# Kernel optimization log

Measured on AMD Instinct MI355X. Metric: run time of the kernel, lower is better.

Reference implementation:

```python
import jax, jax.numpy as jnp
import numpy as np

T, H, E, K, I = 8192, 1024, 8, 2, 512  # tokens, hidden, experts, top_k, expert_intermediate
IS = I * 1  # shared-expert intermediate = expert_intermediate_size * num_shared_experts


def setup_inputs() -> dict:
    key = jax.random.key(0)
    ks = jax.random.split(key, 6)
    s = lambda *d: 1.0 / np.sqrt(d[0])
    return {
        "hidden_states": jax.random.normal(ks[0], (T, H), dtype=jnp.float32),
        "w_gate": jax.random.normal(ks[1], (H, E), dtype=jnp.float32) * s(H),
        "w_experts_gate_up": jax.random.normal(ks[2], (E, H, 2 * I), dtype=jnp.float32) * s(H),
        "w_experts_down": jax.random.normal(ks[3], (E, I, H), dtype=jnp.float32) * s(I),
        "w_shared_gate_up": jax.random.normal(ks[4], (H, 2 * IS), dtype=jnp.float32) * s(H),
        "w_shared_down": jax.random.normal(ks[5], (IS, H), dtype=jnp.float32) * s(IS),
    }


def _silu_and_mul(gu):
    d = gu.shape[-1] // 2
    return jax.nn.silu(gu[..., :d]) * gu[..., d:]


def reference(hidden_states, w_gate, w_experts_gate_up, w_experts_down,
              w_shared_gate_up, w_shared_down):
    x = hidden_states  # [T, H]

    # shared expert: SwiGLU MLP (reduce_results=False path)
    shared_out = _silu_and_mul(x @ w_shared_gate_up) @ w_shared_down  # [T, H]

    # router gate + top-k with renormalization (norm_expert_prob=True)
    router_logits = x @ w_gate  # [T, E]
    probs = jax.nn.softmax(router_logits.astype(jnp.float32), axis=-1)
    topk_w, topk_idx = jax.lax.top_k(probs, K)  # [T, K]
    topk_w = topk_w / jnp.sum(topk_w, axis=-1, keepdims=True)
    # scatter top-k weights into a sparse [T, E] combine matrix
    full_w = jnp.zeros((T, E), dtype=x.dtype)
    full_w = full_w.at[jnp.arange(T)[:, None], topk_idx].set(topk_w.astype(x.dtype))

    # expert SwiGLU MLPs (grouped GEMM expressed as batched einsum over experts)
    gu = jnp.einsum('th,ehi->eti', x, w_experts_gate_up)       # [E, T, 2I]
    act = _silu_and_mul(gu)                                     # [E, T, I]
    expert_out = jnp.einsum('eti,eih->eth', act, w_experts_down)  # [E, T, H]

    # weighted combine over selected experts (weights are zero elsewhere)
    moe_out = jnp.einsum('te,eth->th', full_w, expert_out)     # [T, H]

    return moe_out + shared_out
```

## Files before the change

kernel.cpp:

```cpp
#include <hip/hip_runtime.h>
#include <hip/hip_bf16.h>
#include <cstdint>

#define T_TOK 8192
#define HID   1024
#define NE    9
#define ISZ   512
#define RBASE 18432
#define NSLOT (RBASE + T_TOK)

#define BM 256
#define NROWB (NSLOT / BM)

typedef unsigned short u16;
typedef unsigned int   u32;
typedef signed char    i8;
typedef __attribute__((ext_vector_type(8))) short short8;
typedef __attribute__((ext_vector_type(4))) float f32x4;
typedef __attribute__((ext_vector_type(4))) int   i32x4;

__device__ __forceinline__ u16 f2bf(float f) {
  u32 u = __builtin_bit_cast(u32, f);
  return (u16)((u + 0x7fffu + ((u >> 16) & 1u)) >> 16);
}
__device__ __forceinline__ float bf2f(u16 v) {
  return __builtin_bit_cast(float, (u32)v << 16);
}
__device__ __forceinline__ int q8(float v, float inv) {
  int q = (int)__builtin_rintf(v * inv);
  return (q > 127) ? 127 : ((q < -127) ? -127 : q);
}
__device__ __forceinline__ int colp_of(int c) {
  int i = (c < 512) ? c : (c - 512);
  return (i >> 4) * 32 + ((c < 512) ? 0 : 16) + (i & 15);
}

#define STAGE(gp, lp) __builtin_amdgcn_global_load_lds( \
    (__attribute__((address_space(1))) u32*)(gp),       \
    (__attribute__((address_space(3))) u32*)(lp), 16, 0, 0)

__global__ __launch_bounds__(256) void k_wamax_part(
    const float* __restrict__ wgu, const float* __restrict__ wsg,
    float* __restrict__ pmax) {
  const int e = blockIdx.y, hb = blockIdx.x;
  const float* src = (e < 8) ? (wgu + (size_t)e * 1048576) : wsg;
  const int wv = threadIdx.x >> 6, l = threadIdx.x & 63;
  float4 m4[4];
#pragma unroll
  for (int j = 0; j < 4; ++j) m4[j] = make_float4(0.f, 0.f, 0.f, 0.f);
  const int r0 = hb * 16 + wv * 4;
#pragma unroll
  for (int r = 0; r < 4; ++r) {
    const float* row = src + (size_t)(r0 + r) * 1024;
#pragma unroll
    for (int j = 0; j < 4; ++j) {
      const float4 v = *(const float4*)&row[j * 256 + l * 4];
      m4[j].x = fmaxf(m4[j].x, fabsf(v.x));
      m4[j].y = fmaxf(m4[j].y, fabsf(v.y));
      m4[j].z = fmaxf(m4[j].z, fabsf(v.z));
      m4[j].w = fmaxf(m4[j].w, fabsf(v.w));
    }
  }
  __shared__ float4 red[4][4][64];
#pragma unroll
  for (int j = 0; j < 4; ++j) red[wv][j][l] = m4[j];
  __syncthreads();
  const int j2 = threadIdx.x >> 6, l2 = threadIdx.x & 63;
  const float4 a = red[0][j2][l2], b = red[1][j2][l2];
  const float4 c = red[2][j2][l2], d = red[3][j2][l2];
  float4 o;
  o.x = fmaxf(fmaxf(a.x, b.x), fmaxf(c.x, d.x));
  o.y = fmaxf(fmaxf(a.y, b.y), fmaxf(c.y, d.y));
  o.z = fmaxf(fmaxf(a.z, b.z), fmaxf(c.z, d.z));
  o.w = fmaxf(fmaxf(a.w, b.w), fmaxf(c.w, d.w));
  *(float4*)&pmax[((size_t)e * 64 + hb) * 1024 + j2 * 256 + l2 * 4] = o;
}

__global__ __launch_bounds__(256) void k_wamax_red(
    const float* __restrict__ pmax, float* __restrict__ swc) {
  const int flat = blockIdx.x * 256 + threadIdx.x;
  const int e = flat >> 10, c = flat & 1023;
  float m = 0.f;
  for (int hb = 0; hb < 64; ++hb)
    m = fmaxf(m, pmax[((size_t)e * 64 + hb) * 1024 + c]);
  swc[e * 1024 + colp_of(c)] = m * (1.f / 127.f);
}

#define NB_WGUP (32 * 8 * NE)
#define NB_WDN  (32 * 4 * NE)
#define NB_RTR  (T_TOK / 4)

__global__ __launch_bounds__(256) void k_prep(
    const float* __restrict__ x, const float* __restrict__ wg,
    const float* __restrict__ wgu, const float* __restrict__ wsg,
    const float* __restrict__ wdn, const float* __restrict__ wsd,
    const float* __restrict__ swc,
    i8* __restrict__ xq, float* __restrict__ sxg,
    i8* __restrict__ wguq, u16* __restrict__ wdT,
    int* __restrict__ eidx, float2* __restrict__ wts) {
  __shared__ float tile[32][129];
  const int b = blockIdx.x;
  const int tid = threadIdx.x;

  if (b < NB_WGUP) {
    const int e = b / 256, rem = b % 256;
    const int c0 = (rem & 31) * 32, h0 = (rem >> 5) * 128;
    const float* src = (e < 8) ? (wgu + (size_t)e * HID * 1024) : wsg;
    const int hl = tid >> 1, cb = (tid & 1) * 16;
#pragma unroll
    for (int j = 0; j < 4; ++j) {
      const float4 v = *(const float4*)&src[(size_t)(h0 + hl) * 1024 + c0 + cb + j * 4];
      tile[cb + j * 4 + 0][hl] = v.x;
      tile[cb + j * 4 + 1][hl] = v.y;
      tile[cb + j * 4 + 2][hl] = v.z;
      tile[cb + j * 4 + 3][hl] = v.w;
    }
    __syncthreads();
    const int cl = tid >> 3, hb = (tid & 7) * 16;
    const int cp = colp_of(c0 + cl);
    const float inv = 1.f / swc[e * 1024 + cp];
    i8 out[16];
#pragma unroll
    for (int k = 0; k < 16; ++k) out[k] = (i8)q8(tile[cl][hb + k], inv);
    *(int4*)&wguq[((size_t)e * 1024 + cp) * 1024 + h0 + hb] = *(int4*)out;
    return;
  }
  if (b < NB_WGUP + NB_WDN) {
    const int bb = b - NB_WGUP;
    const int e = bb / 128, r2 = bb % 128;
    const int h0 = (r2 & 31) * 32, i0 = (r2 >> 5) * 128;
    const float* src = (e < 8) ? (wdn + (size_t)e * ISZ * HID) : wsd;
    const int il = tid >> 1, hb2 = (tid & 1) * 16;
#pragma unroll
    for (int j = 0; j < 4; ++j) {
      const float4 v = *(const float4*)&src[(size_t)(i0 + il) * 1024 + h0 + hb2 + j * 4];
      tile[hb2 + j * 4 + 0][il] = v.x;
      tile[hb2 + j * 4 + 1][il] = v.y;
      tile[hb2 + j * 4 + 2][il] = v.z;
      tile[hb2 + j * 4 + 3][il] = v.w;
    }
    __syncthreads();
    const int hl2 = tid >> 3, ib = (tid & 7) * 16;
    u16 ob[16];
#pragma unroll
    for (int k = 0; k < 16; ++k) ob[k] = f2bf(tile[hl2][ib + k]);
    u16* dst = &wdT[((size_t)e * HID + h0 + hl2) * ISZ + i0 + ib];
    *(int4*)dst = *(int4*)ob;
    *(int4*)(dst + 8) = *(int4*)(ob + 8);
    return;
  }
  const int t = (b - NB_WGUP - NB_WDN) * 4 + (tid >> 6);
  const int l = tid & 63;
  float a[8] = {0, 0, 0, 0, 0, 0, 0, 0};
  float vals[16];
  float am = 0.f;
  const float4* xr4 = (const float4*)(x + (size_t)t * HID);
#pragma unroll
  for (int j = 0; j < 4; ++j) {
    const float4 v = xr4[j * 64 + l];
    vals[4 * j] = v.x; vals[4 * j + 1] = v.y; vals[4 * j + 2] = v.z; vals[4 * j + 3] = v.w;
    am = fmaxf(am, fmaxf(fmaxf(fabsf(v.x), fabsf(v.y)), fmaxf(fabsf(v.z), fabsf(v.w))));
    const int h = (j * 64 + l) * 4;
#pragma unroll
    for (int i = 0; i < 4; ++i) {
      const float4 w0 = *(const float4*)&wg[(h + i) * 8];
      const float4 w1 = *(const float4*)&wg[(h + i) * 8 + 4];
      const float ev = vals[4 * j + i];
      a[0] += ev * w0.x; a[1] += ev * w0.y; a[2] += ev * w0.z; a[3] += ev * w0.w;
      a[4] += ev * w1.x; a[5] += ev * w1.y; a[6] += ev * w1.z; a[7] += ev * w1.w;
    }
  }
#pragma unroll
  for (int off = 32; off >= 1; off >>= 1) {
    am = fmaxf(am, __shfl_xor(am, off));
#pragma unroll
    for (int e2 = 0; e2 < 8; ++e2) a[e2] += __shfl_xor(a[e2], off);
  }
  const float inv = (am > 0.f) ? 127.f / am : 0.f;
  u32* xq4 = (u32*)(xq + (size_t)t * HID);
#pragma unroll
  for (int j = 0; j < 4; ++j) {
    u32 q = ((u32)(unsigned char)(i8)q8(vals[4 * j], inv)) |
            ((u32)(unsigned char)(i8)q8(vals[4 * j + 1], inv) << 8) |
            ((u32)(unsigned char)(i8)q8(vals[4 * j + 2], inv) << 16) |
            ((u32)(unsigned char)(i8)q8(vals[4 * j + 3], inv) << 24);
    xq4[j * 64 + l] = q;
  }
  if (l == 0) {
    sxg[t] = am * (1.f / 127.f);
    int ia = 0;
#pragma unroll
    for (int e2 = 1; e2 < 8; ++e2) if (a[e2] > a[ia]) ia = e2;
    int ib = (ia == 0) ? 1 : 0;
#pragma unroll
    for (int e2 = 0; e2 < 8; ++e2) if (e2 != ia && a[e2] > a[ib]) ib = e2;
    float wa = 1.f / (1.f + expf(a[ib] - a[ia]));
    eidx[t] = ia | (ib << 8);
    wts[t] = make_float2(wa, 1.f - wa);
  }
}

__global__ __launch_bounds__(512) void k_scatter(
    const int* __restrict__ eidx, int* __restrict__ btok, int* __restrict__ slotmap,
    int* __restrict__ seg, int* __restrict__ segcnt) {
  __shared__ int cnt_s[8];
  __shared__ int goff_s[9];
  const int e = threadIdx.x >> 6;
  const int l = threadIdx.x & 63;

  int c1 = 0;
  for (int c = 0; c < T_TOK / 64; ++c) {
    int v = eidx[c * 64 + l];
    c1 += __popcll(__ballot((v & 255) == e)) + __popcll(__ballot(((v >> 8) & 255) == e));
  }
  if (l == 0) cnt_s[e] = c1;
  __syncthreads();
  if (threadIdx.x == 0) {
    int off = 0;
    for (int k = 0; k < 8; ++k) { goff_s[k] = off; off += (cnt_s[k] + 255) & ~255; }
    goff_s[8] = off;
  }
  __syncthreads();
  const int base0 = goff_s[e];
  const int cnt_e = cnt_s[e];
  const unsigned long long below = (l == 63) ? ~0ull >> 1 : ((1ull << l) - 1);

  int base = base0;
  for (int c = 0; c < T_TOK / 64; ++c) {
    const int t = c * 64 + l;
    const int v = eidx[t];
    const unsigned long long ma = __ballot((v & 255) == e);
    const unsigned long long mb = __ballot(((v >> 8) & 255) == e);
    if ((v & 255) == e) {
      int s = base + __popcll(ma & below);
      btok[s] = t; slotmap[2 * t] = s;
    }
    if (((v >> 8) & 255) == e) {
      int s = base + __popcll(ma) + __popcll(mb & below);
      btok[s] = t; slotmap[2 * t + 1] = s;
    }
    base += __popcll(ma) + __popcll(mb);
  }
  for (int p = cnt_e + l; p < ((cnt_e + 255) & ~255); p += 64) btok[base0 + p] = 0;
  if (threadIdx.x < 9) seg[threadIdx.x] = goff_s[threadIdx.x];
  if (threadIdx.x < 8) segcnt[threadIdx.x] = cnt_s[threadIdx.x];
}

__device__ __forceinline__ bool seg_lookup(const int* __restrict__ seg,
                                           const int* __restrict__ segcnt,
                                           int brow, int& e) {
  if (brow >= RBASE) { e = 8; return true; }
  if (brow >= seg[8]) return false;
  e = 0;
#pragma unroll
  for (int k = 1; k < 8; ++k) if (brow >= seg[k]) e = k;
  return brow < seg[e] + segcnt[e];
}


#define G1_STG(kt) do { const int _r = ((kt) & 1) * 32768;          \
    STAGE(sA0 + (kt) * 128, Ab + _r + 0 * 8192 + w * 1024);         \
    STAGE(sA1 + (kt) * 128, Ab + _r + 1 * 8192 + w * 1024);         \
    STAGE(sA2 + (kt) * 128, Ab + _r + 2 * 8192 + w * 1024);         \
    STAGE(sA3 + (kt) * 128, Ab + _r + 3 * 8192 + w * 1024);         \
    STAGE(sB0 + (kt) * 128, Bb + _r + 0 * 8192 + w * 1024);         \
    STAGE(sB1 + (kt) * 128, Bb + _r + 1 * 8192 + w * 1024);         \
    STAGE(sB2 + (kt) * 128, Bb + _r + 2 * 8192 + w * 1024);         \
    STAGE(sB3 + (kt) * 128, Bb + _r + 3 * 8192 + w * 1024); } while (0)

#define G1_LOADF(RG, KX) do {                                       \
    _Pragma("unroll") for (int m = 0; m < 4; ++m)                   \
      fA[m] = *(const i32x4*)&Ab[(RG) * 32768 + aBase + m * 2048 + (KX)]; \
    _Pragma("unroll") for (int n = 0; n < 8; ++n)                   \
      fB[n] = *(const i32x4*)&Bb[(RG) * 32768 + bBase + n * 2048 + (KX)]; } while (0)

#define G1_MFMA do { __builtin_amdgcn_s_setprio(1);                 \
    _Pragma("unroll") for (int m = 0; m < 4; ++m)                   \
      _Pragma("unroll") for (int n = 0; n < 8; ++n)                 \
        acc[m][n] = __builtin_amdgcn_mfma_i32_16x16x64_i8(fA[m], fB[n], acc[m][n], 0, 0, 0); \
    __builtin_amdgcn_s_setprio(0); } while (0)

__global__ __launch_bounds__(512) void k_gemm_gu(
    const i8* __restrict__ xq,
    const i8* __restrict__ wguq,
    const int* __restrict__ seg, const int* __restrict__ segcnt,
    const int* __restrict__ btok, const float* __restrict__ sxg,
    const float* __restrict__ swc,
    u16* __restrict__ act)
{
  const int bid = blockIdx.x;
  const int brow = (bid % NROWB) * BM;
  const int bcol = (bid / NROWB) * 256;
  int e;
  if (!seg_lookup(seg, segcnt, brow, e)) return;

  __shared__ __align__(16) i8 Ab[2 * 32768];
  __shared__ __align__(16) i8 Bb[2 * 32768];
  __shared__ float sxl[BM];
  __shared__ float swcl[256];

  const int tid = threadIdx.x;
  const int w = tid >> 6, l = tid & 63;
  const int wm = w >> 1, wn = w & 1;
  const int fr = l & 15, fg = l >> 4;

  if (tid < BM) {
    const int rrow = brow + tid;
    const int tk = (e < 8) ? btok[rrow] : (rrow - RBASE);
    sxl[tid] = sxg[tk];
  } else {
    swcl[tid - 256] = swc[e * 1024 + bcol + (tid - 256)];
  }

  const int rr = w * 8 + (l >> 3);
  const int sw = ((l & 7) ^ (l >> 3)) * 16;
  int tr[4];
#pragma unroll
  for (int j = 0; j < 4; ++j) {
    const int gr = brow + j * 64 + rr;
    tr[j] = (e < 8) ? btok[gr] : (gr - RBASE);
  }
  const i8* sA0 = xq + (size_t)tr[0] * HID + sw;
  const i8* sA1 = xq + (size_t)tr[1] * HID + sw;
  const i8* sA2 = xq + (size_t)tr[2] * HID + sw;
  const i8* sA3 = xq + (size_t)tr[3] * HID + sw;
  const i8* sB0 = wguq + ((size_t)e * 1024 + bcol + 0 * 64 + rr) * HID + sw;
  const i8* sB1 = wguq + ((size_t)e * 1024 + bcol + 1 * 64 + rr) * HID + sw;
  const i8* sB2 = wguq + ((size_t)e * 1024 + bcol + 2 * 64 + rr) * HID + sw;
  const i8* sB3 = wguq + ((size_t)e * 1024 + bcol + 3 * 64 + rr) * HID + sw;

  const int aBase = (wm * 64 + fr) * 128;
  const int bBase = (wn * 128 + fr) * 128;
  const int kx0 = (fg ^ (fr & 7)) * 16;
  const int kx1 = kx0 ^ 64;

  i32x4 acc[4][8];
#pragma unroll
  for (int m = 0; m < 4; ++m)
#pragma unroll
    for (int n = 0; n < 8; ++n) acc[m][n] = (i32x4){0, 0, 0, 0};
  i32x4 fA[4], fB[8];

  const int NKT = HID / 128;
  G1_STG(0);
  asm volatile("s_waitcnt vmcnt(0)" ::: "memory");
  __builtin_amdgcn_s_barrier();
  for (int s = 0; s < NKT; ++s) {
    const int rg = s & 1;
    if (s + 1 < NKT) G1_STG(s + 1);
    G1_LOADF(rg, kx0);
    asm volatile("s_waitcnt lgkmcnt(0)" ::: "memory");
    __builtin_amdgcn_sched_barrier(0);
    G1_MFMA;
    G1_LOADF(rg, kx1);
    asm volatile("s_waitcnt lgkmcnt(0)" ::: "memory");
    __builtin_amdgcn_sched_barrier(0);
    G1_MFMA;
    asm volatile("s_waitcnt vmcnt(0)" ::: "memory");
    __builtin_amdgcn_s_barrier();
  }

#pragma unroll
  for (int m = 0; m < 4; ++m) {
#pragma unroll
    for (int p = 0; p < 4; ++p) {
      const i32x4 gI = acc[m][2 * p], uI = acc[m][2 * p + 1];
      const int col = ((bcol + wn * 128) >> 1) + p * 16 + fr;
      const float swg = swcl[wn * 128 + p * 32 + fr];
      const float swu = swcl[wn * 128 + p * 32 + 16 + fr];
#pragma unroll
      for (int r = 0; r < 4; ++r) {
        const int row_l = wm * 64 + m * 16 + fg * 4 + r;
        const float sx = sxl[row_l];
        const float gate = (float)gI[r] * (sx * swg);
        const float up   = (float)uI[r] * (sx * swu);
        const float sv = gate / (1.f + __expf(-gate));
        act[(size_t)(brow + row_l) * ISZ + col] = f2bf(sv * up);
      }
    }
  }
}


#define D_STGA(kt) do { const int _d = ((kt) % 3) * 8192 + w * 1024; \
    STAGE(dA0 + (kt) * 32, As + _d);                                 \
    STAGE(dA1 + (kt) * 32, As + _d + 512); } while (0)
#define D_STGB(kt) do { const int _d = ((kt) % 3) * 8192 + w * 1024; \
    STAGE(dB0 + (kt) * 32, Bs + _d);                                 \
    STAGE(dB1 + (kt) * 32, Bs + _d + 512); } while (0)
#define D_LDA4(sl, mb) do {                                          \
    af[0] = *(const short8*)&As[(sl) + aOff + ((mb) + 0) * 512];     \
    af[1] = *(const short8*)&As[(sl) + aOff + ((mb) + 1) * 512];     \
    af[2] = *(const short8*)&As[(sl) + aOff + ((mb) + 2) * 512];     \
    af[3] = *(const short8*)&As[(sl) + aOff + ((mb) + 3) * 512]; } while (0)
#define D_LDB4(sl) do {                                              \
    bf[0] = *(const short8*)&Bs[(sl) + bOff + 0 * 512];              \
    bf[1] = *(const short8*)&Bs[(sl) + bOff + 1 * 512];              \
    bf[2] = *(const short8*)&Bs[(sl) + bOff + 2 * 512];              \
    bf[3] = *(const short8*)&Bs[(sl) + bOff + 3 * 512]; } while (0)
#define D_MFMA16(mb) do { __builtin_amdgcn_s_setprio(1);             \
    _Pragma("unroll") for (int mm = 0; mm < 4; ++mm)                 \
      _Pragma("unroll") for (int nn = 0; nn < 4; ++nn)               \
        accf[(mb) + mm][nn] = __builtin_amdgcn_mfma_f32_16x16x32_bf16( \
            af[mm], bf[nn], accf[(mb) + mm][nn], 0, 0, 0);           \
    __builtin_amdgcn_s_setprio(0); } while (0)

__global__ __launch_bounds__(512) void k_gemm_down(
    const u16* __restrict__ act, const u16* __restrict__ wdT,
    const int* __restrict__ seg, const int* __restrict__ segcnt,
    u16* __restrict__ tmp) {
  const int brow = blockIdx.x * BM;
  const int bcol = blockIdx.y * 256;
  int e;
  if (!seg_lookup(seg, segcnt, brow, e)) return;

  __shared__ __align__(16) u16 As[3 * 8192];
  __shared__ __align__(16) u16 Bs[3 * 8192];

  const int tid = threadIdx.x;
  const int w = tid >> 6, l = tid & 63;
  const int wm = w >> 2, wn = w & 3;
  const int fr = l & 15, fg = l >> 4;

  const int arow0 = (w * 128 + l) >> 2;
  const int swd = ((l & 3) ^ (arow0 & 3)) * 8;
  const u16* dA0 = act + (size_t)(brow + arow0) * ISZ + swd;
  const u16* dA1 = act + (size_t)(brow + arow0 + 16) * ISZ + swd;
  const u16* dB0 = wdT + ((size_t)e * 1024 + bcol + arow0) * ISZ + swd;
  const u16* dB1 = wdT + ((size_t)e * 1024 + bcol + arow0 + 16) * ISZ + swd;

  const int aOff = (wm * 128 + fr) * 32 + ((fg ^ (fr & 3)) * 8);
  const int bOff = (wn * 64 + fr) * 32 + ((fg ^ (fr & 3)) * 8);

  f32x4 accf[8][4];
#pragma unroll
  for (int m = 0; m < 8; ++m)
#pragma unroll
    for (int n = 0; n < 4; ++n) accf[m][n] = (f32x4){0.f, 0.f, 0.f, 0.f};
  short8 af[4], bf[4];

  const int NKT = ISZ / 32;
  D_STGA(0); D_STGB(0); D_STGA(1); D_STGB(1);
  asm volatile("s_waitcnt vmcnt(4)" ::: "memory");
  __builtin_amdgcn_s_barrier();
  for (int kt = 0; kt < NKT; ++kt) {
    const int sl = (kt % 3) * 8192;
    D_LDA4(sl, 0); D_LDB4(sl);
    if (kt + 2 < NKT) D_STGA(kt + 2);
    __builtin_amdgcn_s_barrier();
    asm volatile("s_waitcnt lgkmcnt(0)" ::: "memory");
    __builtin_amdgcn_sched_barrier(0);
    D_MFMA16(0);
    __builtin_amdgcn_s_barrier();
    D_LDA4(sl, 4);
    if (kt + 2 < NKT) D_STGB(kt + 2);
    __builtin_amdgcn_s_barrier();
    asm volatile("s_waitcnt lgkmcnt(0)" ::: "memory");
    __builtin_amdgcn_sched_barrier(0);
    D_MFMA16(4);
    if (kt + 2 < NKT)      { asm volatile("s_waitcnt vmcnt(4)" ::: "memory"); }
    else if (kt + 1 < NKT) { asm volatile("s_waitcnt vmcnt(0)" ::: "memory"); }
    __builtin_amdgcn_s_barrier();
  }

#pragma unroll
  for (int m = 0; m < 8; ++m) {
#pragma unroll
    for (int r = 0; r < 4; ++r) {
      const int row = brow + wm * 128 + m * 16 + fg * 4 + r;
#pragma unroll
      for (int n = 0; n < 4; ++n) {
        const int col = bcol + wn * 64 + n * 16 + fr;
        tmp[(size_t)row * HID + col] = f2bf(accf[m][n][r]);
      }
    }
  }
}

__global__ __launch_bounds__(256) void k_combine(
    const u16* __restrict__ tmp, const int* __restrict__ slotmap,
    const float2* __restrict__ wts, float* __restrict__ out) {
  const int idx = blockIdx.x * 256 + threadIdx.x;
  const int t = idx >> 7;
  const int c = (idx & 127) << 3;
  const int s0 = slotmap[2 * t], s1 = slotmap[2 * t + 1];
  const float2 wv = wts[t];
  const short8 a = *(const short8*)(tmp + (size_t)s0 * HID + c);
  const short8 b = *(const short8*)(tmp + (size_t)s1 * HID + c);
  const short8 s = *(const short8*)(tmp + (size_t)(RBASE + t) * HID + c);
  float r[8];
#pragma unroll
  for (int j = 0; j < 8; ++j)
    r[j] = bf2f((u16)s[j]) + wv.x * bf2f((u16)a[j]) + wv.y * bf2f((u16)b[j]);
  float* po = out + (size_t)t * HID + c;
  *(float4*)po       = make_float4(r[0], r[1], r[2], r[3]);
  *(float4*)(po + 4) = make_float4(r[4], r[5], r[6], r[7]);
}

extern "C" void kernel_launch(void* const* d_in, const int* in_sizes, int n_in,
                              void* d_out, int out_size, void* d_ws, size_t ws_size,
                              hipStream_t stream) {
  const float* x   = (const float*)d_in[0];
  const float* wg  = (const float*)d_in[1];
  const float* wgu = (const float*)d_in[2];
  const float* wdn = (const float*)d_in[3];
  const float* wsg = (const float*)d_in[4];
  const float* wsd = (const float*)d_in[5];
  float* out = (float*)d_out;

  char* ws = (char*)d_ws;
  i8*  xq    = (i8*)ws;   ws += (size_t)T_TOK * HID;
  i8*  wguq  = (i8*)ws;   ws += (size_t)NE * 1024 * HID;
  u16* wdT   = (u16*)ws;  ws += (size_t)NE * HID * ISZ * 2;
  u16* actb  = (u16*)ws;  ws += (size_t)NSLOT * ISZ * 2;
  u16* tmp   = (u16*)ws;  ws += (size_t)NSLOT * HID * 2;
  float* sxg = (float*)ws; ws += (size_t)T_TOK * 4;
  float* swc = (float*)ws; ws += (size_t)NE * 1024 * 4;
  float* pmx = (float*)ws; ws += (size_t)NE * 64 * 1024 * 4;
  int* eidx  = (int*)ws;  ws += (size_t)T_TOK * 4;
  float2* wt = (float2*)ws; ws += (size_t)T_TOK * 8;
  int* btok  = (int*)ws;  ws += (size_t)RBASE * 4;
  int* smap  = (int*)ws;  ws += (size_t)2 * T_TOK * 4;
  int* seg   = (int*)ws;  ws += 16 * 4;
  int* segc  = (int*)ws;

  k_wamax_part<<<dim3(64, NE), 256, 0, stream>>>(wgu, wsg, pmx);
  k_wamax_red<<<(NE * 1024) / 256, 256, 0, stream>>>(pmx, swc);
  k_prep<<<NB_WGUP + NB_WDN + NB_RTR, 256, 0, stream>>>(
      x, wg, wgu, wsg, wdn, wsd, swc, xq, sxg, wguq, wdT, eidx, wt);
  k_scatter<<<1, 512, 0, stream>>>(eidx, btok, smap, seg, segc);
  k_gemm_gu<<<NROWB * 4, 512, 0, stream>>>(
      xq, wguq, seg, segc, btok, sxg, swc, actb);
  k_gemm_down<<<dim3(NROWB, HID / 256), 512, 0, stream>>>(actb, wdT, seg, segc, tmp);
  k_combine<<<(T_TOK * HID / 8) / 256, 256, 0, stream>>>(tmp, smap, wt, out);
}
```

Measured before the change: 206.3 us.

## Restructure down-projection GEMM to BK=64 double-buffered pipeline with 4x2 warp layout

The down-projection GEMM moves from a 3-stage ring with K-tiles of 32 to a 2-stage double buffer with K-tiles of 64. It uses an 8-way XOR swizzle and a 4x2 warp grid, giving each wave 64x128 instead of 128x64. Barriers per K-step drop from four to one, and the grid becomes 1D with row blocks varying fastest, presumably so blocks that share a weight column tile run together. In exchange there is less prefetch depth: each stage waits on vmcnt(0), so global latency may be exposed more.

```diff
diff --git a/kernel.cpp b/kernel.cpp
--- a/kernel.cpp
+++ b/kernel.cpp
@@ -382,95 +382,97 @@
 }
 
 
-#define D_STGA(kt) do { const int _d = ((kt) % 3) * 8192 + w * 1024; \
-    STAGE(dA0 + (kt) * 32, As + _d);                                 \
-    STAGE(dA1 + (kt) * 32, As + _d + 512); } while (0)
-#define D_STGB(kt) do { const int _d = ((kt) % 3) * 8192 + w * 1024; \
-    STAGE(dB0 + (kt) * 32, Bs + _d);                                 \
-    STAGE(dB1 + (kt) * 32, Bs + _d + 512); } while (0)
-#define D_LDA4(sl, mb) do {                                          \
-    af[0] = *(const short8*)&As[(sl) + aOff + ((mb) + 0) * 512];     \
-    af[1] = *(const short8*)&As[(sl) + aOff + ((mb) + 1) * 512];     \
-    af[2] = *(const short8*)&As[(sl) + aOff + ((mb) + 2) * 512];     \
-    af[3] = *(const short8*)&As[(sl) + aOff + ((mb) + 3) * 512]; } while (0)
-#define D_LDB4(sl) do {                                              \
-    bf[0] = *(const short8*)&Bs[(sl) + bOff + 0 * 512];              \
-    bf[1] = *(const short8*)&Bs[(sl) + bOff + 1 * 512];              \
-    bf[2] = *(const short8*)&Bs[(sl) + bOff + 2 * 512];              \
-    bf[3] = *(const short8*)&Bs[(sl) + bOff + 3 * 512]; } while (0)
-#define D_MFMA16(mb) do { __builtin_amdgcn_s_setprio(1);             \
-    _Pragma("unroll") for (int mm = 0; mm < 4; ++mm)                 \
-      _Pragma("unroll") for (int nn = 0; nn < 4; ++nn)               \
-        accf[(mb) + mm][nn] = __builtin_amdgcn_mfma_f32_16x16x32_bf16( \
-            af[mm], bf[nn], accf[(mb) + mm][nn], 0, 0, 0);           \
+#define G2_STG(kt) do { const int _r = ((kt) & 1) * 16384;          \
+    STAGE(dA0 + (kt) * 64, As2 + _r + 0 * 4096 + w * 512);          \
+    STAGE(dA1 + (kt) * 64, As2 + _r + 1 * 4096 + w * 512);          \
+    STAGE(dA2 + (kt) * 64, As2 + _r + 2 * 4096 + w * 512);          \
+    STAGE(dA3 + (kt) * 64, As2 + _r + 3 * 4096 + w * 512);          \
+    STAGE(dB0 + (kt) * 64, Bs2 + _r + 0 * 4096 + w * 512);          \
+    STAGE(dB1 + (kt) * 64, Bs2 + _r + 1 * 4096 + w * 512);          \
+    STAGE(dB2 + (kt) * 64, Bs2 + _r + 2 * 4096 + w * 512);          \
+    STAGE(dB3 + (kt) * 64, Bs2 + _r + 3 * 4096 + w * 512); } while (0)
+
+#define G2_LOADF(RG, KX) do {                                       \
+    _Pragma("unroll") for (int m = 0; m < 4; ++m)                   \
+      gA[m] = *(const short8*)&As2[(RG) * 16384 + aBase + m * 1024 + (KX)]; \
+    _Pragma("unroll") for (int n = 0; n < 8; ++n)                   \
+      gB[n] = *(const short8*)&Bs2[(RG) * 16384 + bBase + n * 1024 + (KX)]; } while (0)
+
+#define G2_MFMA do { __builtin_amdgcn_s_setprio(1);                 \
+    _Pragma("unroll") for (int m = 0; m < 4; ++m)                   \
+      _Pragma("unroll") for (int n = 0; n < 8; ++n)                 \
+        accf[m][n] = __builtin_amdgcn_mfma_f32_16x16x32_bf16(gA[m], gB[n], accf[m][n], 0, 0, 0); \
     __builtin_amdgcn_s_setprio(0); } while (0)
 
 __global__ __launch_bounds__(512) void k_gemm_down(
-    const u16* __restrict__ act, const u16* __restrict__ wdT,
+    const u16* __restrict__ act,
+    const u16* __restrict__ wdT,
     const int* __restrict__ seg, const int* __restrict__ segcnt,
     u16* __restrict__ tmp) {
-  const int brow = blockIdx.x * BM;
-  const int bcol = blockIdx.y * 256;
+  const int bid = blockIdx.x;
+  const int brow = (bid % NROWB) * BM;
+  const int bcol = (bid / NROWB) * 256;
   int e;
   if (!seg_lookup(seg, segcnt, brow, e)) return;
 
-  __shared__ __align__(16) u16 As[3 * 8192];
-  __shared__ __align__(16) u16 Bs[3 * 8192];
+  __shared__ __align__(16) u16 As2[2 * 16384];
+  __shared__ __align__(16) u16 Bs2[2 * 16384];
 
   const int tid = threadIdx.x;
   const int w = tid >> 6, l = tid & 63;
-  const int wm = w >> 2, wn = w & 3;
+  const int wm = w >> 1, wn = w & 1;
   const int fr = l & 15, fg = l >> 4;
 
-  const int arow0 = (w * 128 + l) >> 2;
-  const int swd = ((l & 3) ^ (arow0 & 3)) * 8;
-  const u16* dA0 = act + (size_t)(brow + arow0) * ISZ + swd;
-  const u16* dA1 = act + (size_t)(brow + arow0 + 16) * ISZ + swd;
-  const u16* dB0 = wdT + ((size_t)e * 1024 + bcol + arow0) * ISZ + swd;
-  const u16* dB1 = wdT + ((size_t)e * 1024 + bcol + arow0 + 16) * ISZ + swd;
-
-  const int aOff = (wm * 128 + fr) * 32 + ((fg ^ (fr & 3)) * 8);
-  const int bOff = (wn * 64 + fr) * 32 + ((fg ^ (fr & 3)) * 8);
-
-  f32x4 accf[8][4];
-#pragma unroll
-  for (int m = 0; m < 8; ++m)
-#pragma unroll
-    for (int n = 0; n < 4; ++n) accf[m][n] = (f32x4){0.f, 0.f, 0.f, 0.f};
-  short8 af[4], bf[4];
-
-  const int NKT = ISZ / 32;
-  D_STGA(0); D_STGB(0); D_STGA(1); D_STGB(1);
-  asm volatile("s_waitcnt vmcnt(4)" ::: "memory");
+  const int rr = w * 8 + (l >> 3);
+  const int sw = ((l & 7) ^ (l >> 3)) * 8;
+  const u16* dA0 = act + (size_t)(brow + 0 * 64 + rr) * ISZ + sw;
+  const u16* dA1 = act + (size_t)(brow + 1 * 64 + rr) * ISZ + sw;
+  const u16* dA2 = act + (size_t)(brow + 2 * 64 + rr) * ISZ + sw;
+  const u16* dA3 = act + (size_t)(brow + 3 * 64 + rr) * ISZ + sw;
+  const u16* dB0 = wdT + ((size_t)e * 1024 + bcol + 0 * 64 + rr) * ISZ + sw;
+  const u16* dB1 = wdT + ((size_t)e * 1024 + bcol + 1 * 64 + rr) * ISZ + sw;
+  const u16* dB2 = wdT + ((size_t)e * 1024 + bcol + 2 * 64 + rr) * ISZ + sw;
+  const u16* dB3 = wdT + ((size_t)e * 1024 + bcol + 3 * 64 + rr) * ISZ + sw;
+
+  const int aBase = (wm * 64 + fr) * 64;
+  const int bBase = (wn * 128 + fr) * 64;
+  const int kx0 = (fg ^ (fr & 7)) * 8;
+  const int kx1 = kx0 ^ 32;
+
+  f32x4 accf[4][8];
+#pragma unroll
+  for (int m = 0; m < 4; ++m)
+#pragma unroll
+    for (int n = 0; n < 8; ++n) accf[m][n] = (f32x4){0.f, 0.f, 0.f, 0.f};
+  short8 gA[4], gB[8];
+
+  const int NKT = ISZ / 64;
+  G2_STG(0);
+  asm volatile("s_waitcnt vmcnt(0)" ::: "memory");
   __builtin_amdgcn_s_barrier();
-  for (int kt = 0; kt < NKT; ++kt) {
-    const int sl = (kt % 3) * 8192;
-    D_LDA4(sl, 0); D_LDB4(sl);
-    if (kt + 2 < NKT) D_STGA(kt + 2);
-    __builtin_amdgcn_s_barrier();
+  for (int s = 0; s < NKT; ++s) {
+    const int rg = s & 1;
+    if (s + 1 < NKT) G2_STG(s + 1);
+    G2_LOADF(rg, kx0);
     asm volatile("s_waitcnt lgkmcnt(0)" ::: "memory");
     __builtin_amdgcn_sched_barrier(0);
-    D_MFMA16(0);
-    __builtin_amdgcn_s_barrier();
-    D_LDA4(sl, 4);
-    if (kt + 2 < NKT) D_STGB(kt + 2);
-    __builtin_amdgcn_s_barrier();
+    G2_MFMA;
+    G2_LOADF(rg, kx1);
     asm volatile("s_waitcnt lgkmcnt(0)" ::: "memory");
     __builtin_amdgcn_sched_barrier(0);
-    D_MFMA16(4);
-    if (kt + 2 < NKT)      { asm volatile("s_waitcnt vmcnt(4)" ::: "memory"); }
-    else if (kt + 1 < NKT) { asm volatile("s_waitcnt vmcnt(0)" ::: "memory"); }
+    G2_MFMA;
+    asm volatile("s_waitcnt vmcnt(0)" ::: "memory");
     __builtin_amdgcn_s_barrier();
   }
 
 #pragma unroll
-  for (int m = 0; m < 8; ++m) {
+  for (int m = 0; m < 4; ++m) {
 #pragma unroll
     for (int r = 0; r < 4; ++r) {
-      const int row = brow + wm * 128 + m * 16 + fg * 4 + r;
-#pragma unroll
-      for (int n = 0; n < 4; ++n) {
-        const int col = bcol + wn * 64 + n * 16 + fr;
+      const int row = brow + wm * 64 + m * 16 + fg * 4 + r;
+#pragma unroll
+      for (int n = 0; n < 8; ++n) {
+        const int col = bcol + wn * 128 + n * 16 + fr;
         tmp[(size_t)row * HID + col] = f2bf(accf[m][n][r]);
       }
     }
@@ -531,6 +533,6 @@
   k_scatter<<<1, 512, 0, stream>>>(eidx, btok, smap, seg, segc);
   k_gemm_gu<<<NROWB * 4, 512, 0, stream>>>(
       xq, wguq, seg, segc, btok, sxg, swc, actb);
-  k_gemm_down<<<dim3(NROWB, HID / 256), 512, 0, stream>>>(actb, wdT, seg, segc, tmp);
+  k_gemm_down<<<NROWB * 4, 512, 0, stream>>>(actb, wdT, seg, segc, tmp);
   k_combine<<<(T_TOK * HID / 8) / 256, 256, 0, stream>>>(tmp, smap, wt, out);
 }
```

Result: no change. 202.5 us (-1.9%).
